# Optimization experiments

Hardware: AMD Instinct MI355X
Metric: run time of the kernel (lower is better)

## Reference

```python
import jax, jax.numpy as jnp
import numpy as np

D = 256      # d_model
H = 8        # n_heads
L = 4        # n_levels
P = 4        # n_points
DFF = 1024   # d_ffn
DH = D // H  # head dim
SPATIAL = np.array([[100, 100], [50, 50], [25, 25], [13, 13]], dtype=np.int64)  # (H_l, W_l)
LV = int((SPATIAL[:, 0] * SPATIAL[:, 1]).sum())  # 13294 flattened memory tokens


def layer_norm(x, w, b, eps=1e-5):
    m = jnp.mean(x, -1, keepdims=True)
    v = jnp.mean((x - m) ** 2, -1, keepdims=True)
    return (x - m) * jax.lax.rsqrt(v + eps) * w + b


def setup_inputs() -> dict:
    key = jax.random.key(0)
    ks = jax.random.split(key, 16)
    nq, bs = 900, 8

    def w(k, shape, s=0.02):
        return jax.random.normal(k, shape, dtype=jnp.float32) * s

    return {
        "tgt": jax.random.normal(ks[0], (nq, bs, D), jnp.float32),
        "tgt_query_pos": jax.random.normal(ks[1], (nq, bs, D), jnp.float32),
        "tgt_reference_points": jax.random.uniform(ks[2], (nq, bs, L, 2), jnp.float32),
        "memory": jax.random.normal(ks[3], (LV, bs, D), jnp.float32),
        "sa_Wqkv": w(ks[4], (3 * D, D)), "sa_bqkv": jnp.zeros((3 * D,), jnp.float32),
        "sa_Wo": w(ks[5], (D, D)), "sa_bo": jnp.zeros((D,), jnp.float32),
        "ln1_w": jnp.ones((D,), jnp.float32), "ln1_b": jnp.zeros((D,), jnp.float32),
        "ln2_w": jnp.ones((D,), jnp.float32), "ln2_b": jnp.zeros((D,), jnp.float32),
        "ln3_w": jnp.ones((D,), jnp.float32), "ln3_b": jnp.zeros((D,), jnp.float32),
        "ca_Woff": w(ks[6], (H * L * P * 2, D)), "ca_boff": w(ks[7], (H * L * P * 2,), 0.5),
        "ca_Wattn": w(ks[8], (H * L * P, D)), "ca_battn": jnp.zeros((H * L * P,), jnp.float32),
        "ca_Wval": w(ks[9], (D, D)), "ca_bval": jnp.zeros((D,), jnp.float32),
        "ca_Wout": w(ks[10], (D, D)), "ca_bout": jnp.zeros((D,), jnp.float32),
        "ffn_W1": w(ks[11], (DFF, D)), "ffn_b1": jnp.zeros((DFF,), jnp.float32),
        "ffn_W2": w(ks[12], (D, DFF)), "ffn_b2": jnp.zeros((D,), jnp.float32),
        "memory_key_padding_mask": jnp.zeros((bs, LV), jnp.bool_),
        "memory_spatial_shapes": jnp.asarray(SPATIAL),
    }


def msdeform_attn(query, ref, value, mask, shapes_np,
                  Woff, boff, Wattn, battn, Wval, bval, Wout, bout):
    # query: [bs,nq,D], ref: [bs,nq,L,2], value: [bs,lv,D], mask: [bs,lv]
    bs, nq, _ = query.shape
    lv = value.shape[1]
    v = value @ Wval.T + bval
    v = jnp.where(mask[:, :, None], 0.0, v)
    v = v.reshape(bs, lv, H, DH).transpose(0, 2, 1, 3)  # [bs,H,lv,DH]
    off = (query @ Woff.T + boff).reshape(bs, nq, H, L, P, 2)
    aw = jax.nn.softmax((query @ Wattn.T + battn).reshape(bs, nq, H, L * P), -1)
    aw = aw.reshape(bs, nq, H, L, P)
    # offset normalizer is [W_l, H_l]
    norm = jnp.asarray(shapes_np[:, ::-1].copy(), jnp.float32)  # [L,2]
    loc = ref[:, :, None, :, None, :] + off / norm[None, None, None, :, None, :]
    out = jnp.zeros((bs, nq, H, DH), jnp.float32)
    start = 0
    for l in range(L):
        Hl, Wl = int(shapes_np[l, 0]), int(shapes_np[l, 1])
        vf = v[:, :, start:start + Hl * Wl]  # [bs,H,Hl*Wl,DH]
        start += Hl * Wl
        # grid_sample(align_corners=False) pixel coords
        x = loc[:, :, :, l, :, 0] * Wl - 0.5  # [bs,nq,H,P]
        y = loc[:, :, :, l, :, 1] * Hl - 0.5
        x0 = jnp.floor(x); y0 = jnp.floor(y)
        fx = x - x0; fy = y - y0
        x0i = x0.astype(jnp.int32); y0i = y0.astype(jnp.int32)

        def gather(yi, xi):
            valid = ((xi >= 0) & (xi < Wl) & (yi >= 0) & (yi < Hl)).astype(jnp.float32)
            idx = jnp.clip(yi, 0, Hl - 1) * Wl + jnp.clip(xi, 0, Wl - 1)
            idx_t = idx.transpose(0, 2, 1, 3).reshape(bs, H, nq * P, 1)
            g = jnp.take_along_axis(vf, idx_t, axis=2)  # [bs,H,nq*P,DH]
            return g * valid.transpose(0, 2, 1, 3).reshape(bs, H, nq * P, 1)

        def wgt(w):
            return w.transpose(0, 2, 1, 3).reshape(bs, H, nq * P, 1)

        samp = (gather(y0i, x0i) * wgt((1 - fx) * (1 - fy))
                + gather(y0i, x0i + 1) * wgt(fx * (1 - fy))
                + gather(y0i + 1, x0i) * wgt((1 - fx) * fy)
                + gather(y0i + 1, x0i + 1) * wgt(fx * fy))
        samp = samp.reshape(bs, H, nq, P, DH)
        out = out + jnp.einsum('bhqpd,bqhp->bqhd', samp, aw[:, :, :, l])
    return out.reshape(bs, nq, D) @ Wout.T + bout


def reference(tgt, tgt_query_pos, tgt_reference_points, memory,
              sa_Wqkv, sa_bqkv, sa_Wo, sa_bo,
              ln1_w, ln1_b, ln2_w, ln2_b, ln3_w, ln3_b,
              ca_Woff, ca_boff, ca_Wattn, ca_battn, ca_Wval, ca_bval, ca_Wout, ca_bout,
              ffn_W1, ffn_b1, ffn_W2, ffn_b2,
              memory_key_padding_mask, memory_spatial_shapes):
    shapes_np = np.asarray(memory_spatial_shapes)  # static per trace
    nq, bs, _ = tgt.shape
    # --- self attention (post-LN, residual) ---
    q = tgt + tgt_query_pos
    qp = (q @ sa_Wqkv[:D].T + sa_bqkv[:D]).reshape(nq, bs, H, DH)
    kp = (q @ sa_Wqkv[D:2 * D].T + sa_bqkv[D:2 * D]).reshape(nq, bs, H, DH)
    vp = (tgt @ sa_Wqkv[2 * D:].T + sa_bqkv[2 * D:]).reshape(nq, bs, H, DH)
    scores = jnp.einsum('qbhd,kbhd->bhqk', qp, kp) * (1.0 / float(np.sqrt(DH)))
    attn = jax.nn.softmax(scores, -1)
    o = jnp.einsum('bhqk,kbhd->qbhd', attn, vp).reshape(nq, bs, D) @ sa_Wo.T + sa_bo
    tgt = layer_norm(tgt + o, ln2_w, ln2_b)
    # --- multi-scale deformable cross attention ---
    query = (tgt + tgt_query_pos).transpose(1, 0, 2)      # [bs,nq,D]
    ref = tgt_reference_points.transpose(1, 0, 2, 3)      # [bs,nq,L,2]
    val = memory.transpose(1, 0, 2)                       # [bs,lv,D]
    ca = msdeform_attn(query, ref, val, memory_key_padding_mask, shapes_np,
                       ca_Woff, ca_boff, ca_Wattn, ca_battn,
                       ca_Wval, ca_bval, ca_Wout, ca_bout).transpose(1, 0, 2)
    tgt = layer_norm(tgt + ca, ln1_w, ln1_b)
    # --- FFN ---
    t2 = jax.nn.relu(tgt @ ffn_W1.T + ffn_b1) @ ffn_W2.T + ffn_b2
    return layer_norm(tgt + t2, ln3_w, ln3_b)
```

## Files before the change

### kernel.cpp

```cpp
#include <hip/hip_runtime.h>
#include <hip/hip_bf16.h>

#define NQ   900
#define BSZ  8
#define DM   256
#define NH   8
#define DHD  32
#define DFF_ 1024
#define LVTOT 13294
#define NTOK (NQ*BSZ)
#define MVAL (LVTOT*BSZ)

typedef __attribute__((ext_vector_type(8))) short bf16x8;
typedef __attribute__((ext_vector_type(4))) short bf16x4;
typedef __attribute__((ext_vector_type(4))) float f32x4;
typedef unsigned int u32;

__device__ __forceinline__ unsigned short f2bf(float x) {
  union { __hip_bfloat16 h; unsigned short u; } cv;
  cv.h = __float2bfloat16(x);
  return cv.u;
}
__device__ __forceinline__ float bf2f(unsigned short u) {
  union { __hip_bfloat16 h; unsigned short u; } cv;
  cv.u = u;
  return __bfloat162float(cv.h);
}

__device__ __forceinline__ void gl_lds16(const void* gsrc, void* ldst) {
  __builtin_amdgcn_global_load_lds(
      (const __attribute__((address_space(1))) u32*)gsrc,
      (__attribute__((address_space(3))) u32*)ldst, 16, 0, 0);
}

__global__ __launch_bounds__(256) void addcast_kernel(const float* __restrict__ a,
                                                      const float* __restrict__ b,
                                                      unsigned short* __restrict__ o, int n8) {
  int i = blockIdx.x * 256 + threadIdx.x;
  if (i >= n8) return;
  float4 a0 = ((const float4*)a)[i * 2], a1 = ((const float4*)a)[i * 2 + 1];
  float4 b0 = ((const float4*)b)[i * 2], b1 = ((const float4*)b)[i * 2 + 1];
  bf16x8 v;
  v[0] = (short)f2bf(a0.x + b0.x); v[1] = (short)f2bf(a0.y + b0.y);
  v[2] = (short)f2bf(a0.z + b0.z); v[3] = (short)f2bf(a0.w + b0.w);
  v[4] = (short)f2bf(a1.x + b1.x); v[5] = (short)f2bf(a1.y + b1.y);
  v[6] = (short)f2bf(a1.z + b1.z); v[7] = (short)f2bf(a1.w + b1.w);
  *(bf16x8*)(o + (long)i * 8) = v;
}

__global__ __launch_bounds__(256) void cast_weights_kernel(
    const float* p0, const float* p1, const float* p2, const float* p3,
    const float* p4, const float* p5, const float* p6, const float* p7,
    unsigned short* dst) {
  long i8 = ((long)blockIdx.x * 256 + threadIdx.x) * 8;
  if (i8 >= 1015808) return;
  const float* src; long off;
  if      (i8 < 196608) { src = p0; off = i8; }
  else if (i8 < 262144) { src = p1; off = i8 - 196608; }
  else if (i8 < 327680) { src = p2; off = i8 - 262144; }
  else if (i8 < 393216) { src = p3; off = i8 - 327680; }
  else if (i8 < 425984) { src = p4; off = i8 - 393216; }
  else if (i8 < 491520) { src = p5; off = i8 - 425984; }
  else if (i8 < 753664) { src = p6; off = i8 - 491520; }
  else                  { src = p7; off = i8 - 753664; }
  float4 a = *(const float4*)(src + off);
  float4 b = *(const float4*)(src + off + 4);
  bf16x8 v;
  v[0] = (short)f2bf(a.x); v[1] = (short)f2bf(a.y);
  v[2] = (short)f2bf(a.z); v[3] = (short)f2bf(a.w);
  v[4] = (short)f2bf(b.x); v[5] = (short)f2bf(b.y);
  v[6] = (short)f2bf(b.z); v[7] = (short)f2bf(b.w);
  *(bf16x8*)(dst + i8) = v;
}

__global__ __launch_bounds__(256) void concat_bias_kernel(const float* __restrict__ a,
                                                          const float* __restrict__ b,
                                                          float* __restrict__ o) {
  int i = blockIdx.x * 256 + threadIdx.x;
  if (i < 256) o[i] = a[i];
  else if (i < 384) o[i] = b[i - 256];
}

template <int AF32, int OUT_BF16, int RELU, int NSTEP>
__global__ __launch_bounds__(256, 4) void gemm_s_kernel(
    const void* __restrict__ Araw, const unsigned short* __restrict__ W,
    const float* __restrict__ bias, void* __restrict__ C,
    int M, int ldc) {
  constexpr int K = NSTEP * 64;
  constexpr int ABYTES = AF32 ? 32768 : 16384;
  __shared__ alignas(16) unsigned char As[ABYTES];
  __shared__ alignas(16) unsigned char Bs[16384];
  int tid = threadIdx.x;
  int l = tid & 63, w = tid >> 6;
  int lr = l & 15, lg = l >> 4;
  int wr = w >> 1, wc = w & 1;
  int n0 = blockIdx.x * 128, m0 = blockIdx.y * 128;
  int phase = blockIdx.y & (NSTEP - 1);

  f32x4 acc[4][4];
#pragma unroll
  for (int m = 0; m < 4; m++)
#pragma unroll
    for (int n = 0; n < 4; n++) acc[m][n] = (f32x4){0.f, 0.f, 0.f, 0.f};

  for (int tt = 0; tt < NSTEP; tt++) {
    int t = tt + phase; if (t >= NSTEP) t -= NSTEP;
    int k0 = t * 64;
    __syncthreads();
#pragma unroll
    for (int i4 = 0; i4 < 4; i4++) {
      int i = i4 * 4 + w;
      int row = i * 8 + (l >> 3);
      int sc = (l & 7) ^ (row & 7);
      gl_lds16(W + (long)(n0 + row) * K + k0 + sc * 8, Bs + i * 1024 + l * 16);
    }
    if (AF32) {
      const float* Af = (const float*)Araw;
#pragma unroll
      for (int i4 = 0; i4 < 8; i4++) {
        int i = i4 * 4 + w;
        int row = i * 4 + (l >> 4);
        int g = m0 + row; if (g >= M) g = M - 1;
        int sc = (l & 15) ^ (row & 15);
        gl_lds16(Af + (long)g * K + k0 + sc * 4, As + i * 1024 + l * 16);
      }
    } else {
      const unsigned short* A = (const unsigned short*)Araw;
#pragma unroll
      for (int i4 = 0; i4 < 4; i4++) {
        int i = i4 * 4 + w;
        int row = i * 8 + (l >> 3);
        int g = m0 + row; if (g >= M) g = M - 1;
        int sc = (l & 7) ^ (row & 7);
        gl_lds16(A + (long)g * K + k0 + sc * 8, As + i * 1024 + l * 16);
      }
    }
    __syncthreads();

#pragma unroll
    for (int sk = 0; sk < 2; sk++) {
      bf16x8 af[4], bfr[4];
      if (AF32) {
#pragma unroll
        for (int m = 0; m < 4; m++) {
          int row = wr * 64 + m * 16 + lr;
          int ca = (sk * 8 + lg * 2) ^ (row & 15);
          int cb = (sk * 8 + lg * 2 + 1) ^ (row & 15);
          f32x4 fa = *(const f32x4*)(As + row * 256 + ca * 16);
          f32x4 fb = *(const f32x4*)(As + row * 256 + cb * 16);
          bf16x8 v;
          v[0] = (short)f2bf(fa[0]); v[1] = (short)f2bf(fa[1]);
          v[2] = (short)f2bf(fa[2]); v[3] = (short)f2bf(fa[3]);
          v[4] = (short)f2bf(fb[0]); v[5] = (short)f2bf(fb[1]);
          v[6] = (short)f2bf(fb[2]); v[7] = (short)f2bf(fb[3]);
          af[m] = v;
        }
      } else {
#pragma unroll
        for (int m = 0; m < 4; m++) {
          int row = wr * 64 + m * 16 + lr;
          int c = (sk * 4 + lg) ^ (row & 7);
          af[m] = *(const bf16x8*)(As + row * 128 + c * 16);
        }
      }
#pragma unroll
      for (int n = 0; n < 4; n++) {
        int row = wc * 64 + n * 16 + lr;
        int c = (sk * 4 + lg) ^ (row & 7);
        bfr[n] = *(const bf16x8*)(Bs + row * 128 + c * 16);
      }
#pragma unroll
      for (int m = 0; m < 4; m++)
#pragma unroll
        for (int n = 0; n < 4; n++)
          acc[m][n] = __builtin_amdgcn_mfma_f32_16x16x32_bf16(af[m], bfr[n], acc[m][n], 0, 0, 0);
    }
  }

  float bv[4];
#pragma unroll
  for (int ni = 0; ni < 4; ni++) bv[ni] = bias[n0 + wc * 64 + ni * 16 + lr];
#pragma unroll
  for (int mi = 0; mi < 4; mi++) {
#pragma unroll
    for (int r = 0; r < 4; r++) {
      int row = m0 + wr * 64 + mi * 16 + lg * 4 + r;
      if (row < M) {
#pragma unroll
        for (int ni = 0; ni < 4; ni++) {
          int col = n0 + wc * 64 + ni * 16 + lr;
          float v = acc[mi][ni][r] + bv[ni];
          if (RELU) v = fmaxf(v, 0.f);
          if (OUT_BF16) ((unsigned short*)C)[(long)row * ldc + col] = f2bf(v);
          else          ((float*)C)[(long)row * ldc + col] = v;
        }
      }
    }
  }
}

__global__ __launch_bounds__(256) void attn_mfma_kernel(const unsigned short* __restrict__ qkv,
                                                        unsigned short* __restrict__ out) {
  __shared__ unsigned short Vt[32][72];
  __shared__ unsigned short Ps[4][16][72];
  int tid = threadIdx.x;
  int l = tid & 63, w = tid >> 6;
  int lr = l & 15, lg = l >> 4;
  int q0 = blockIdx.x * 64;
  int h = blockIdx.y & 7, b = blockIdx.y >> 3;
  const float scale = 0.17677669529663687f;

  int qrow = q0 + w * 16 + lr;
  int qclamp = qrow < 899 ? qrow : 899;
  bf16x8 qf = *(const bf16x8*)(qkv + ((long)qclamp * 8 + b) * 768 + h * 32 + lg * 8);

  f32x4 o_acc[2];
  o_acc[0] = (f32x4){0.f, 0.f, 0.f, 0.f};
  o_acc[1] = (f32x4){0.f, 0.f, 0.f, 0.f};
  float m_run[4] = {-1e30f, -1e30f, -1e30f, -1e30f};
  float l_run[4] = {0.f, 0.f, 0.f, 0.f};

  for (int k0 = 0; k0 < NQ; k0 += 64) {
    __syncthreads();
    {
      int key = tid >> 2, dg = tid & 3;
      int kk = k0 + key; if (kk > 899) kk = 899;
      bf16x8 vv = *(const bf16x8*)(qkv + ((long)kk * 8 + b) * 768 + 512 + h * 32 + dg * 8);
#pragma unroll
      for (int j = 0; j < 8; j++) Vt[dg * 8 + j][key] = (unsigned short)vv[j];
    }
    f32x4 sg[4];
#pragma unroll
    for (int ng = 0; ng < 4; ng++) {
      int key = k0 + ng * 16 + lr; int kc = key < 899 ? key : 899;
      bf16x8 kf = *(const bf16x8*)(qkv + ((long)kc * 8 + b) * 768 + 256 + h * 32 + lg * 8);
      sg[ng] = __builtin_amdgcn_mfma_f32_16x16x32_bf16(qf, kf, (f32x4){0.f, 0.f, 0.f, 0.f}, 0, 0, 0);
    }
    float sv[4][4];
#pragma unroll
    for (int ng = 0; ng < 4; ng++) {
      bool bad = (k0 + ng * 16 + lr) >= NQ;
#pragma unroll
      for (int r = 0; r < 4; r++) sv[ng][r] = bad ? -1e30f : sg[ng][r] * scale;
    }
    float p[4][4];
#pragma unroll
    for (int r = 0; r < 4; r++) {
      float rmax = fmaxf(fmaxf(sv[0][r], sv[1][r]), fmaxf(sv[2][r], sv[3][r]));
#pragma unroll
      for (int mk = 8; mk; mk >>= 1) rmax = fmaxf(rmax, __shfl_xor(rmax, mk));
      float mnew = fmaxf(m_run[r], rmax);
      float fs = __expf(m_run[r] - mnew);
      m_run[r] = mnew;
      float ps = 0.f;
#pragma unroll
      for (int ng = 0; ng < 4; ng++) { p[ng][r] = __expf(sv[ng][r] - mnew); ps += p[ng][r]; }
#pragma unroll
      for (int mk = 8; mk; mk >>= 1) ps += __shfl_xor(ps, mk);
      l_run[r] = l_run[r] * fs + ps;
      o_acc[0][r] *= fs;
      o_acc[1][r] *= fs;
    }
#pragma unroll
    for (int ng = 0; ng < 4; ng++)
#pragma unroll
      for (int r = 0; r < 4; r++)
        Ps[w][lg * 4 + r][lr + ng * 16] = f2bf(p[ng][r]);
    __syncthreads();
#pragma unroll
    for (int ks = 0; ks < 2; ks++) {
      bf16x8 pf = *(const bf16x8*)&Ps[w][lr][ks * 32 + lg * 8];
#pragma unroll
      for (int ni = 0; ni < 2; ni++) {
        bf16x8 vf = *(const bf16x8*)&Vt[ni * 16 + lr][ks * 32 + lg * 8];
        o_acc[ni] = __builtin_amdgcn_mfma_f32_16x16x32_bf16(pf, vf, o_acc[ni], 0, 0, 0);
      }
    }
  }
#pragma unroll
  for (int r = 0; r < 4; r++) {
    int orow = q0 + w * 16 + lg * 4 + r;
    if (orow < NQ) {
      float inv = 1.f / l_run[r];
      unsigned short* op = out + ((long)orow * 8 + b) * 256 + h * 32 + lr;
      op[0]  = f2bf(o_acc[0][r] * inv);
      op[16] = f2bf(o_acc[1][r] * inv);
    }
  }
}

__device__ __forceinline__ void fetch8_acc(const unsigned short* __restrict__ vtmp, int lo, int W,
                                           int yi, int xi, int b, int col0, float wgt,
                                           float* a) {
  if ((xi < 0) | (xi >= W) | (yi < 0) | (yi >= W)) return;
  const unsigned short* p = vtmp + ((long)((lo + yi * W + xi) * BSZ + b)) * 256 + col0;
  bf16x8 r = *(const bf16x8*)p;
#pragma unroll
  for (int j = 0; j < 8; j++) a[j] += wgt * bf2f((unsigned short)r[j]);
}

__global__ __launch_bounds__(256) void sampler_kernel(const unsigned short* __restrict__ vtmp,
                                                      const float* __restrict__ oa,
                                                      const float* __restrict__ ref,
                                                      unsigned short* __restrict__ samp) {
  __shared__ float s_off[8][256];
  __shared__ float s_aw[8][128];
  __shared__ float s_ref[8][8];
  int tid = threadIdx.x;
  int t0 = blockIdx.x * 8;
#pragma unroll
  for (int k = 0; k < 8; k++) s_off[k][tid] = oa[(long)(t0 + k) * 384 + tid];
#pragma unroll
  for (int i = 0; i < 4; i++) {
    int idx = i * 256 + tid;
    int k = idx >> 7, c = idx & 127;
    s_aw[k][c] = oa[(long)(t0 + k) * 384 + 256 + c];
  }
  if (tid < 64) s_ref[tid >> 3][tid & 7] = ref[(long)(t0 + (tid >> 3)) * 8 + (tid & 7)];
  __syncthreads();
  if (tid < 64) {
    int k = tid >> 3, hh = tid & 7;
    float* p = &s_aw[k][hh * 16];
    float m = -1e30f;
#pragma unroll
    for (int j = 0; j < 16; j++) m = fmaxf(m, p[j]);
    float s = 0.f;
#pragma unroll
    for (int j = 0; j < 16; j++) { p[j] = __expf(p[j] - m); s += p[j]; }
    float inv = 1.f / s;
#pragma unroll
    for (int j = 0; j < 16; j++) p[j] *= inv;
  }
  __syncthreads();
  int w = tid >> 5;
  int l = tid & 31;
  int t = t0 + w;
  int h = l >> 2, col0 = h * 32 + (l & 3) * 8;
  int b = t & 7;
  const int Wls[4]  = {100, 50, 25, 13};
  const int lofs[4] = {0, 10000, 12500, 13125};
  float a[8];
#pragma unroll
  for (int j = 0; j < 8; j++) a[j] = 0.f;
#pragma unroll
  for (int lvl = 0; lvl < 4; lvl++) {
    int W = Wls[lvl];
    float Wf = (float)W;
    int lo = lofs[lvl];
    float rx = s_ref[w][lvl * 2 + 0], ry = s_ref[w][lvl * 2 + 1];
#pragma unroll
    for (int p = 0; p < 4; p++) {
      float ox = s_off[w][((h * 4 + lvl) * 4 + p) * 2 + 0];
      float oy = s_off[w][((h * 4 + lvl) * 4 + p) * 2 + 1];
      float x = rx * Wf + ox - 0.5f;
      float y = ry * Wf + oy - 0.5f;
      float x0f = floorf(x), y0f = floorf(y);
      float fx = x - x0f, fy = y - y0f;
      int x0 = (int)x0f, y0 = (int)y0f;
      float aa = s_aw[w][h * 16 + lvl * 4 + p];
      float w00 = aa * (1.f - fx) * (1.f - fy);
      float w01 = aa * fx * (1.f - fy);
      float w10 = aa * (1.f - fx) * fy;
      float w11 = aa * fx * fy;
      fetch8_acc(vtmp, lo, W, y0,     x0,     b, col0, w00, a);
      fetch8_acc(vtmp, lo, W, y0,     x0 + 1, b, col0, w01, a);
      fetch8_acc(vtmp, lo, W, y0 + 1, x0,     b, col0, w10, a);
      fetch8_acc(vtmp, lo, W, y0 + 1, x0 + 1, b, col0, w11, a);
    }
  }
  bf16x8 o;
#pragma unroll
  for (int j = 0; j < 8; j++) o[j] = (short)f2bf(a[j]);
  *(bf16x8*)(samp + (long)t * 256 + col0) = o;
}

__global__ __launch_bounds__(256) void ln_kernel(const float* __restrict__ x,
                                                 const float* __restrict__ res,
                                                 const float* __restrict__ w,
                                                 const float* __restrict__ bvec,
                                                 float* __restrict__ out,
                                                 unsigned short* __restrict__ out_bf,
                                                 const float* __restrict__ pos,
                                                 unsigned short* __restrict__ pos_bf,
                                                 int rows) {
  int wv = threadIdx.x >> 6, lane = threadIdx.x & 63;
  int row = blockIdx.x * 4 + wv;
  if (row >= rows) return;
  float4 xv = *(const float4*)(x + (long)row * 256 + lane * 4);
  float4 rv = *(const float4*)(res + (long)row * 256 + lane * 4);
  float v0 = xv.x + rv.x, v1 = xv.y + rv.y, v2 = xv.z + rv.z, v3 = xv.w + rv.w;
  float s = v0 + v1 + v2 + v3;
#pragma unroll
  for (int o = 32; o; o >>= 1) s += __shfl_xor(s, o);
  float mean = s * (1.f / 256.f);
  float d0 = v0 - mean, d1 = v1 - mean, d2 = v2 - mean, d3 = v3 - mean;
  float q = d0 * d0 + d1 * d1 + d2 * d2 + d3 * d3;
#pragma unroll
  for (int o = 32; o; o >>= 1) q += __shfl_xor(q, o);
  float rstd = rsqrtf(q * (1.f / 256.f) + 1e-5f);
  float4 wv4 = *(const float4*)(w + lane * 4);
  float4 bv4 = *(const float4*)(bvec + lane * 4);
  float o0 = d0 * rstd * wv4.x + bv4.x;
  float o1 = d1 * rstd * wv4.y + bv4.y;
  float o2 = d2 * rstd * wv4.z + bv4.z;
  float o3 = d3 * rstd * wv4.w + bv4.w;
  *(float4*)(out + (long)row * 256 + lane * 4) = make_float4(o0, o1, o2, o3);
  if (out_bf) {
    unsigned short* p = out_bf + (long)row * 256 + lane * 4;
    p[0] = f2bf(o0); p[1] = f2bf(o1); p[2] = f2bf(o2); p[3] = f2bf(o3);
  }
  if (pos_bf) {
    float4 pv = *(const float4*)(pos + (long)row * 256 + lane * 4);
    unsigned short* p = pos_bf + (long)row * 256 + lane * 4;
    p[0] = f2bf(o0 + pv.x); p[1] = f2bf(o1 + pv.y);
    p[2] = f2bf(o2 + pv.z); p[3] = f2bf(o3 + pv.w);
  }
}

extern "C" void kernel_launch(void* const* d_in, const int* in_sizes, int n_in,
                              void* d_out, int out_size, void* d_ws, size_t ws_size,
                              hipStream_t stream) {
  const float* tgt     = (const float*)d_in[0];
  const float* pos     = (const float*)d_in[1];
  const float* refpts  = (const float*)d_in[2];
  const float* memory  = (const float*)d_in[3];
  const float* sa_Wqkv = (const float*)d_in[4];
  const float* sa_bqkv = (const float*)d_in[5];
  const float* sa_Wo   = (const float*)d_in[6];
  const float* sa_bo   = (const float*)d_in[7];
  const float* ln1_w   = (const float*)d_in[8];
  const float* ln1_b   = (const float*)d_in[9];
  const float* ln2_w   = (const float*)d_in[10];
  const float* ln2_b   = (const float*)d_in[11];
  const float* ln3_w   = (const float*)d_in[12];
  const float* ln3_b   = (const float*)d_in[13];
  const float* ca_Woff = (const float*)d_in[14];
  const float* ca_boff = (const float*)d_in[15];
  const float* ca_Wattn= (const float*)d_in[16];
  const float* ca_battn= (const float*)d_in[17];
  const float* ca_Wval = (const float*)d_in[18];
  const float* ca_bval = (const float*)d_in[19];
  const float* ca_Wout = (const float*)d_in[20];
  const float* ca_bout = (const float*)d_in[21];
  const float* ffn_W1  = (const float*)d_in[22];
  const float* ffn_b1  = (const float*)d_in[23];
  const float* ffn_W2  = (const float*)d_in[24];
  const float* ffn_b2  = (const float*)d_in[25];

  char* ws = (char*)d_ws;
  float*          buf_ca = (float*)(ws);
  float*          buf_t3 = (float*)(ws + 8388608);
  unsigned short* t3_bf  = (unsigned short*)(ws + 16777216);
  unsigned short* buf_h  = (unsigned short*)(ws + 20971520);
  float*          buf_f  = (float*)(ws + 36700160);
  float*          bias_cat = (float*)(ws + 44072960);
  unsigned short* buf_v  = (unsigned short*)(ws + 54452224);
  unsigned short* wts    = (unsigned short*)(ws + 112590848);
  unsigned short* buf_q  = (unsigned short*)(ws + 114622464);
  unsigned short* buf_qkv= (unsigned short*)(ws + 118308864);
  float*          buf_oa = (float*)(ws + 118308864);
  unsigned short* buf_o  = (unsigned short*)(ws + 129368064);
  unsigned short* buf_smp= (unsigned short*)(ws + 129368064);
  float*          buf_t2 = (float*)(ws + 133054464);

  const unsigned short* w_qkv = wts + 0;
  const unsigned short* w_o   = wts + 196608;
  const unsigned short* w_val = wts + 262144;
  const unsigned short* w_oa  = wts + 327680;
  const unsigned short* w_out = wts + 425984;
  const unsigned short* w_f1  = wts + 491520;
  const unsigned short* w_f2  = wts + 753664;

  dim3 blk(256);
  const int n8tok = NTOK * DM / 8;

  cast_weights_kernel<<<(1015808 / 8 + 255) / 256, blk, 0, stream>>>(
      sa_Wqkv, sa_Wo, ca_Wval, ca_Woff, ca_Wattn, ca_Wout, ffn_W1, ffn_W2, wts);
  concat_bias_kernel<<<2, blk, 0, stream>>>(ca_boff, ca_battn, bias_cat);
  addcast_kernel<<<(n8tok + 255) / 256, blk, 0, stream>>>(tgt, pos, buf_q, n8tok);
  gemm_s_kernel<0, 1, 0, 4><<<dim3(4, 57), blk, 0, stream>>>(buf_q, w_qkv, sa_bqkv,
                                                             buf_qkv, NTOK, 768);
  gemm_s_kernel<1, 1, 0, 4><<<dim3(2, 57), blk, 0, stream>>>(tgt, w_qkv + 512 * 256,
                                                             sa_bqkv + 512, buf_qkv + 512,
                                                             NTOK, 768);
  gemm_s_kernel<1, 1, 0, 4><<<dim3(2, 831), blk, 0, stream>>>(memory, w_val, ca_bval,
                                                              buf_v, MVAL, 256);
  attn_mfma_kernel<<<dim3(15, 64), blk, 0, stream>>>(buf_qkv, buf_o);
  gemm_s_kernel<0, 0, 0, 4><<<dim3(2, 57), blk, 0, stream>>>(buf_o, w_o, sa_bo,
                                                             buf_t2, NTOK, 256);
  ln_kernel<<<1800, blk, 0, stream>>>(buf_t2, tgt, ln2_w, ln2_b, buf_t2, nullptr,
                                      pos, buf_q, NTOK);
  gemm_s_kernel<0, 0, 0, 4><<<dim3(3, 57), blk, 0, stream>>>(buf_q, w_oa, bias_cat,
                                                             buf_oa, NTOK, 384);
  sampler_kernel<<<NTOK / 8, blk, 0, stream>>>(buf_v, buf_oa, refpts, buf_smp);
  gemm_s_kernel<0, 0, 0, 4><<<dim3(2, 57), blk, 0, stream>>>(buf_smp, w_out, ca_bout,
                                                             buf_ca, NTOK, 256);
  ln_kernel<<<1800, blk, 0, stream>>>(buf_ca, buf_t2, ln1_w, ln1_b, buf_t3, t3_bf,
                                      nullptr, nullptr, NTOK);
  gemm_s_kernel<0, 1, 1, 4><<<dim3(8, 57), blk, 0, stream>>>(t3_bf, w_f1, ffn_b1,
                                                             buf_h, NTOK, 1024);
  gemm_s_kernel<0, 0, 0, 16><<<dim3(2, 57), blk, 0, stream>>>(buf_h, w_f2, ffn_b2,
                                                              buf_f, NTOK, 256);
  ln_kernel<<<1800, blk, 0, stream>>>(buf_f, buf_t3, ln3_w, ln3_b, (float*)d_out, nullptr,
                                      nullptr, nullptr, NTOK);
}
```

Before: 234.7 us.

## Replace direct global-to-LDS GEMM loads with register-prefetched double-staged tiles

The GEMM kernel no longer uses global_load_lds DMA. Each thread now loads its A/B tile slice into registers one k-step ahead, so the next tile's global loads overlap the current step's MFMA work. For fp32 activations, conversion to bf16 moves from LDS-read time to LDS-write time, halving the A tile's LDS footprint. The cost is higher register pressure (launch bounds lowered from 4 to 3 blocks per CU) and the loss of the asynchronous direct-to-LDS path.

```diff
diff --git a/kernel.cpp b/kernel.cpp
--- a/kernel.cpp
+++ b/kernel.cpp
@@ -25,12 +25,6 @@
   union { __hip_bfloat16 h; unsigned short u; } cv;
   cv.u = u;
   return __bfloat162float(cv.h);
-}
-
-__device__ __forceinline__ void gl_lds16(const void* gsrc, void* ldst) {
-  __builtin_amdgcn_global_load_lds(
-      (const __attribute__((address_space(1))) u32*)gsrc,
-      (__attribute__((address_space(3))) u32*)ldst, 16, 0, 0);
 }
 
 __global__ __launch_bounds__(256) void addcast_kernel(const float* __restrict__ a,
@@ -82,14 +76,13 @@
 }
 
 template <int AF32, int OUT_BF16, int RELU, int NSTEP>
-__global__ __launch_bounds__(256, 4) void gemm_s_kernel(
+__global__ __launch_bounds__(256, 3) void gemm_r_kernel(
     const void* __restrict__ Araw, const unsigned short* __restrict__ W,
     const float* __restrict__ bias, void* __restrict__ C,
     int M, int ldc) {
   constexpr int K = NSTEP * 64;
-  constexpr int ABYTES = AF32 ? 32768 : 16384;
-  __shared__ alignas(16) unsigned char As[ABYTES];
-  __shared__ alignas(16) unsigned char Bs[16384];
+  __shared__ alignas(16) unsigned short As[128 * 64];
+  __shared__ alignas(16) unsigned short Bs[128 * 64];
   int tid = threadIdx.x;
   int l = tid & 63, w = tid >> 6;
   int lr = l & 15, lg = l >> 4;
@@ -97,77 +90,86 @@
   int n0 = blockIdx.x * 128, m0 = blockIdx.y * 128;
   int phase = blockIdx.y & (NSTEP - 1);
 
+  int r = tid >> 1, h = tid & 1;
+  long ga = m0 + r; if (ga >= M) ga = M - 1;
+  long gb = n0 + r;
+  int rw = r & 7;
+
   f32x4 acc[4][4];
 #pragma unroll
   for (int m = 0; m < 4; m++)
 #pragma unroll
     for (int n = 0; n < 4; n++) acc[m][n] = (f32x4){0.f, 0.f, 0.f, 0.f};
+
+  f32x4 va[8];
+  bf16x8 vab[4];
+  bf16x8 vbb[4];
+
+  auto loadA = [&](int k0) {
+    if (AF32) {
+      const float* Af = (const float*)Araw;
+      const float* p = Af + ga * K + k0 + h * 32;
+#pragma unroll
+      for (int j = 0; j < 8; j++) va[j] = *(const f32x4*)(p + j * 4);
+    } else {
+      const unsigned short* A = (const unsigned short*)Araw;
+      const unsigned short* p = A + ga * K + k0 + h * 32;
+#pragma unroll
+      for (int i = 0; i < 4; i++) vab[i] = *(const bf16x8*)(p + i * 8);
+    }
+  };
+  auto loadB = [&](int k0) {
+    const unsigned short* p = W + gb * K + k0 + h * 32;
+#pragma unroll
+    for (int i = 0; i < 4; i++) vbb[i] = *(const bf16x8*)(p + i * 8);
+  };
+  auto writeAB = [&]() {
+#pragma unroll
+    for (int i = 0; i < 4; i++) {
+      int c = h * 4 + i;
+      int s = c ^ rw;
+      bf16x8 v;
+      if (AF32) {
+        f32x4 a0 = va[2 * i], a1 = va[2 * i + 1];
+        v[0] = (short)f2bf(a0[0]); v[1] = (short)f2bf(a0[1]);
+        v[2] = (short)f2bf(a0[2]); v[3] = (short)f2bf(a0[3]);
+        v[4] = (short)f2bf(a1[0]); v[5] = (short)f2bf(a1[1]);
+        v[6] = (short)f2bf(a1[2]); v[7] = (short)f2bf(a1[3]);
+      } else {
+        v = vab[i];
+      }
+      *(bf16x8*)(As + r * 64 + s * 8) = v;
+      *(bf16x8*)(Bs + r * 64 + s * 8) = vbb[i];
+    }
+  };
+
+  loadA(phase * 64);
+  loadB(phase * 64);
 
   for (int tt = 0; tt < NSTEP; tt++) {
     int t = tt + phase; if (t >= NSTEP) t -= NSTEP;
-    int k0 = t * 64;
     __syncthreads();
-#pragma unroll
-    for (int i4 = 0; i4 < 4; i4++) {
-      int i = i4 * 4 + w;
-      int row = i * 8 + (l >> 3);
-      int sc = (l & 7) ^ (row & 7);
-      gl_lds16(W + (long)(n0 + row) * K + k0 + sc * 8, Bs + i * 1024 + l * 16);
-    }
-    if (AF32) {
-      const float* Af = (const float*)Araw;
-#pragma unroll
-      for (int i4 = 0; i4 < 8; i4++) {
-        int i = i4 * 4 + w;
-        int row = i * 4 + (l >> 4);
-        int g = m0 + row; if (g >= M) g = M - 1;
-        int sc = (l & 15) ^ (row & 15);
-        gl_lds16(Af + (long)g * K + k0 + sc * 4, As + i * 1024 + l * 16);
-      }
-    } else {
-      const unsigned short* A = (const unsigned short*)Araw;
-#pragma unroll
-      for (int i4 = 0; i4 < 4; i4++) {
-        int i = i4 * 4 + w;
-        int row = i * 8 + (l >> 3);
-        int g = m0 + row; if (g >= M) g = M - 1;
-        int sc = (l & 7) ^ (row & 7);
-        gl_lds16(A + (long)g * K + k0 + sc * 8, As + i * 1024 + l * 16);
-      }
-    }
+    writeAB();
     __syncthreads();
-
+    if (tt + 1 < NSTEP) {
+      int t2 = tt + 1 + phase; if (t2 >= NSTEP) t2 -= NSTEP;
+      loadA(t2 * 64);
+      loadB(t2 * 64);
+    }
 #pragma unroll
     for (int sk = 0; sk < 2; sk++) {
       bf16x8 af[4], bfr[4];
-      if (AF32) {
-#pragma unroll
-        for (int m = 0; m < 4; m++) {
-          int row = wr * 64 + m * 16 + lr;
-          int ca = (sk * 8 + lg * 2) ^ (row & 15);
-          int cb = (sk * 8 + lg * 2 + 1) ^ (row & 15);
-          f32x4 fa = *(const f32x4*)(As + row * 256 + ca * 16);
-          f32x4 fb = *(const f32x4*)(As + row * 256 + cb * 16);
-          bf16x8 v;
-          v[0] = (short)f2bf(fa[0]); v[1] = (short)f2bf(fa[1]);
-          v[2] = (short)f2bf(fa[2]); v[3] = (short)f2bf(fa[3]);
-          v[4] = (short)f2bf(fb[0]); v[5] = (short)f2bf(fb[1]);
-          v[6] = (short)f2bf(fb[2]); v[7] = (short)f2bf(fb[3]);
-          af[m] = v;
-        }
-      } else {
-#pragma unroll
-        for (int m = 0; m < 4; m++) {
-          int row = wr * 64 + m * 16 + lr;
-          int c = (sk * 4 + lg) ^ (row & 7);
-          af[m] = *(const bf16x8*)(As + row * 128 + c * 16);
-        }
+#pragma unroll
+      for (int m = 0; m < 4; m++) {
+        int row = wr * 64 + m * 16 + lr;
+        int c = (sk * 4 + lg) ^ (row & 7);
+        af[m] = *(const bf16x8*)(As + row * 64 + c * 8);
       }
 #pragma unroll
       for (int n = 0; n < 4; n++) {
         int row = wc * 64 + n * 16 + lr;
         int c = (sk * 4 + lg) ^ (row & 7);
-        bfr[n] = *(const bf16x8*)(Bs + row * 128 + c * 16);
+        bfr[n] = *(const bf16x8*)(Bs + row * 64 + c * 8);
       }
 #pragma unroll
       for (int m = 0; m < 4; m++)
@@ -183,13 +185,13 @@
 #pragma unroll
   for (int mi = 0; mi < 4; mi++) {
 #pragma unroll
-    for (int r = 0; r < 4; r++) {
-      int row = m0 + wr * 64 + mi * 16 + lg * 4 + r;
+    for (int r2 = 0; r2 < 4; r2++) {
+      int row = m0 + wr * 64 + mi * 16 + lg * 4 + r2;
       if (row < M) {
 #pragma unroll
         for (int ni = 0; ni < 4; ni++) {
           int col = n0 + wc * 64 + ni * 16 + lr;
-          float v = acc[mi][ni][r] + bv[ni];
+          float v = acc[mi][ni][r2] + bv[ni];
           if (RELU) v = fmaxf(v, 0.f);
           if (OUT_BF16) ((unsigned short*)C)[(long)row * ldc + col] = f2bf(v);
           else          ((float*)C)[(long)row * ldc + col] = v;
@@ -478,28 +480,28 @@
       sa_Wqkv, sa_Wo, ca_Wval, ca_Woff, ca_Wattn, ca_Wout, ffn_W1, ffn_W2, wts);
   concat_bias_kernel<<<2, blk, 0, stream>>>(ca_boff, ca_battn, bias_cat);
   addcast_kernel<<<(n8tok + 255) / 256, blk, 0, stream>>>(tgt, pos, buf_q, n8tok);
-  gemm_s_kernel<0, 1, 0, 4><<<dim3(4, 57), blk, 0, stream>>>(buf_q, w_qkv, sa_bqkv,
+  gemm_r_kernel<0, 1, 0, 4><<<dim3(4, 57), blk, 0, stream>>>(buf_q, w_qkv, sa_bqkv,
                                                              buf_qkv, NTOK, 768);
-  gemm_s_kernel<1, 1, 0, 4><<<dim3(2, 57), blk, 0, stream>>>(tgt, w_qkv + 512 * 256,
+  gemm_r_kernel<1, 1, 0, 4><<<dim3(2, 57), blk, 0, stream>>>(tgt, w_qkv + 512 * 256,
                                                              sa_bqkv + 512, buf_qkv + 512,
                                                              NTOK, 768);
-  gemm_s_kernel<1, 1, 0, 4><<<dim3(2, 831), blk, 0, stream>>>(memory, w_val, ca_bval,
+  gemm_r_kernel<1, 1, 0, 4><<<dim3(2, 831), blk, 0, stream>>>(memory, w_val, ca_bval,
                                                               buf_v, MVAL, 256);
   attn_mfma_kernel<<<dim3(15, 64), blk, 0, stream>>>(buf_qkv, buf_o);
-  gemm_s_kernel<0, 0, 0, 4><<<dim3(2, 57), blk, 0, stream>>>(buf_o, w_o, sa_bo,
+  gemm_r_kernel<0, 0, 0, 4><<<dim3(2, 57), blk, 0, stream>>>(buf_o, w_o, sa_bo,
                                                              buf_t2, NTOK, 256);
   ln_kernel<<<1800, blk, 0, stream>>>(buf_t2, tgt, ln2_w, ln2_b, buf_t2, nullptr,
                                       pos, buf_q, NTOK);
-  gemm_s_kernel<0, 0, 0, 4><<<dim3(3, 57), blk, 0, stream>>>(buf_q, w_oa, bias_cat,
+  gemm_r_kernel<0, 0, 0, 4><<<dim3(3, 57), blk, 0, stream>>>(buf_q, w_oa, bias_cat,
                                                              buf_oa, NTOK, 384);
   sampler_kernel<<<NTOK / 8, blk, 0, stream>>>(buf_v, buf_oa, refpts, buf_smp);
-  gemm_s_kernel<0, 0, 0, 4><<<dim3(2, 57), blk, 0, stream>>>(buf_smp, w_out, ca_bout,
+  gemm_r_kernel<0, 0, 0, 4><<<dim3(2, 57), blk, 0, stream>>>(buf_smp, w_out, ca_bout,
                                                              buf_ca, NTOK, 256);
   ln_kernel<<<1800, blk, 0, stream>>>(buf_ca, buf_t2, ln1_w, ln1_b, buf_t3, t3_bf,
                                       nullptr, nullptr, NTOK);
-  gemm_s_kernel<0, 1, 1, 4><<<dim3(8, 57), blk, 0, stream>>>(t3_bf, w_f1, ffn_b1,
+  gemm_r_kernel<0, 1, 1, 4><<<dim3(8, 57), blk, 0, stream>>>(t3_bf, w_f1, ffn_b1,
                                                              buf_h, NTOK, 1024);
-  gemm_s_kernel<0, 0, 0, 16><<<dim3(2, 57), blk, 0, stream>>>(buf_h, w_f2, ffn_b2,
+  gemm_r_kernel<0, 0, 0, 16><<<dim3(2, 57), blk, 0, stream>>>(buf_h, w_f2, ffn_b2,
                                                               buf_f, NTOK, 256);
   ln_kernel<<<1800, blk, 0, stream>>>(buf_f, buf_t3, ln3_w, ln3_b, (float*)d_out, nullptr,
                                       nullptr, nullptr, NTOK);
```

New measurement: 253.6 us. 8.1% more time.
